# Optimization experiments

Measured on AMD Instinct MI355X. Metric: run time of the kernel, lower is better.

The kernel has to match this reference:

```python
import jax, jax.numpy as jnp
import numpy as np
import math

B, S, DIM = 1, 2048, 2048
H, KVH, HD = 32, 8, 64
REP = H // KVH


def _rope_cache(seqlen, head_dim, base=10000.0):
    # (seqlen, 2*head_dim): [cos | sin], each duplicated across both halves
    inv_freq = 1.0 / (base ** (np.arange(0, head_dim, 2, dtype=np.float32) / head_dim))
    t = np.arange(seqlen, dtype=np.float32)
    ang = np.outer(t, inv_freq)                    # (S, HD/2)
    ang = np.concatenate([ang, ang], axis=-1)      # (S, HD)
    return jnp.asarray(np.concatenate([np.cos(ang), np.sin(ang)], axis=-1))


def setup_inputs() -> dict:
    key = jax.random.key(0)
    ks = jax.random.split(key, 12)
    std = 0.02
    return {
        "x": jax.random.normal(ks[0], (B, S, DIM), jnp.float32),
        "rope_cache": _rope_cache(S, HD),
        "wq_w": jax.random.normal(ks[1], (H * HD, DIM), jnp.float32) * std,
        "wq_b": jax.random.normal(ks[2], (H * HD,), jnp.float32) * std,
        "wk_w": jax.random.normal(ks[3], (KVH * HD, DIM), jnp.float32) * std,
        "wk_b": jax.random.normal(ks[4], (KVH * HD,), jnp.float32) * std,
        "wv_w": jax.random.normal(ks[5], (KVH * HD, DIM), jnp.float32) * std,
        "wv_b": jax.random.normal(ks[6], (KVH * HD,), jnp.float32) * std,
        "wo_w": jax.random.normal(ks[7], (DIM, H * HD), jnp.float32) * std,
        "wo_b": jax.random.normal(ks[8], (DIM,), jnp.float32) * std,
        "sinks": jax.random.normal(ks[9], (H,), jnp.float32) * std,
    }


def _rotate_half(t):
    h = t.shape[-1] // 2
    return jnp.concatenate([-t[..., h:], t[..., :h]], axis=-1)


def reference(x, rope_cache, wq_w, wq_b, wk_w, wk_b, wv_w, wv_b, wo_w, wo_b, sinks):
    bsz, seqlen, _ = x.shape
    q = (jnp.einsum('bsd,od->bso', x, wq_w) + wq_b).reshape(bsz, seqlen, H, HD)
    k = (jnp.einsum('bsd,od->bso', x, wk_w) + wk_b).reshape(bsz, seqlen, KVH, HD)
    v = (jnp.einsum('bsd,od->bso', x, wv_w) + wv_b).reshape(bsz, seqlen, KVH, HD)

    cos = rope_cache[:seqlen, :HD][None, :, None, :]
    sin = rope_cache[:seqlen, HD:][None, :, None, :]
    q = q * cos + _rotate_half(q) * sin
    k = k * cos + _rotate_half(k) * sin

    # repeat_kv: repeat_interleave along head dim
    k = jnp.repeat(k, REP, axis=2)  # (B,S,H,HD)
    v = jnp.repeat(v, REP, axis=2)

    q = q.transpose(0, 2, 1, 3)  # (B,H,S,HD)
    k = k.transpose(0, 2, 1, 3)
    v = v.transpose(0, 2, 1, 3)

    scale = 1.0 / math.sqrt(HD)
    scores = jnp.einsum('bhqd,bhkd->bhqk', q, k) * scale
    causal = jnp.tril(jnp.ones((seqlen, seqlen), dtype=bool))
    scores = jnp.where(causal, scores, -jnp.inf)

    m = jnp.max(scores, axis=-1, keepdims=True)
    lse = m[..., 0] + jnp.log(jnp.sum(jnp.exp(scores - m), axis=-1))  # (B,H,S)
    attn = jnp.exp(scores - lse[..., None])
    out = jnp.einsum('bhqk,bhkd->bhqd', attn, v)

    # sink-token LSE renormalization
    combined_lse = jnp.logaddexp(lse, sinks[None, :, None])
    renorm = jnp.exp(jnp.clip(lse - combined_lse, -20.0, 0.0))
    out = out * renorm[..., None]

    out = out.transpose(0, 2, 1, 3).reshape(bsz, seqlen, H * HD)
    return jnp.einsum('bso,do->bsd', out, wo_w) + wo_b
```

## Files before the change

### kernel.cpp

```cpp
#include <hip/hip_runtime.h>


#define S_LEN 2048
#define DIM_  2048
#define QK_LD 2560

typedef __attribute__((ext_vector_type(8))) __bf16 bf16x8;
typedef __attribute__((ext_vector_type(4))) float f32x4;
typedef __attribute__((ext_vector_type(4))) unsigned short us4;

__device__ __forceinline__ unsigned short f2bf(float f) {
    union { float f; unsigned u; } v; v.f = f;
    unsigned r = v.u + 0x7FFFu + ((v.u >> 16) & 1u);
    return (unsigned short)(r >> 16);
}
__device__ __forceinline__ float bf2f(unsigned short u) {
    union { unsigned u; float f; } v; v.u = ((unsigned)u) << 16;
    return v.f;
}

__device__ __forceinline__ void gload_lds16(const void* g, void* l) {
    __builtin_amdgcn_global_load_lds(
        (const __attribute__((address_space(1))) void*)g,
        (__attribute__((address_space(3))) void*)l, 16, 0, 0);
}

__device__ __forceinline__ int swz32(int r, int ch) { return r*32 + ((ch ^ ((r >> 1) & 3)) << 3); }
__device__ __forceinline__ int swz64(int r, int ch) { return r*64 + ((ch ^ (r & 7)) << 3); }

__global__ void cvt_all(const float* __restrict__ x,  const float* __restrict__ wq,
                        const float* __restrict__ wk, const float* __restrict__ wv,
                        const float* __restrict__ wo,
                        unsigned short* __restrict__ xb,
                        unsigned short* __restrict__ wqkv,
                        unsigned short* __restrict__ wob) {
    const int i4 = blockIdx.x * 256 + threadIdx.x;
    const float* src; unsigned short* dst; int off;
    if (i4 < 1048576)      { src = x;  dst = xb;             off = i4; }
    else if (i4 < 2097152) { src = wq; dst = wqkv;           off = i4 - 1048576; }
    else if (i4 < 2359296) { src = wk; dst = wqkv + 4194304; off = i4 - 2097152; }
    else if (i4 < 2621440) { src = wv; dst = wqkv + 5242880; off = i4 - 2359296; }
    else                   { src = wo; dst = wob;            off = i4 - 2621440; }
    const float4 v = reinterpret_cast<const float4*>(src)[off];
    us4 o = { f2bf(v.x), f2bf(v.y), f2bf(v.z), f2bf(v.w) };
    reinterpret_cast<us4*>(dst)[off] = o;
}

__global__ void build_bias(const float* __restrict__ qb, const float* __restrict__ kb,
                           const float* __restrict__ vb, float* __restrict__ out) {
    const int i = blockIdx.x * 256 + threadIdx.x;
    if (i < 2048) out[i] = qb[i];
    else if (i < 2560) out[i] = kb[i - 2048];
    else if (i < 3072) out[i] = vb[i - 2560];
}

template<int MODE>
__global__ __launch_bounds__(256)
void gemm_bt(const unsigned short* __restrict__ A,
             const unsigned short* __restrict__ B,
             const float* __restrict__ bias,
             unsigned short* __restrict__ Cqk,
             unsigned short* __restrict__ Vt,
             float* __restrict__ Cf,
             int K)
{
    __shared__ unsigned short As[3][128 * 32];
    __shared__ unsigned short Bs[3][128 * 32];
    const int t = threadIdx.x;
    const int lane = t & 63;
    const int w = t >> 6;
    const int wr = w >> 1, wc = w & 1;
    const int lq = lane & 15;
    const int g = lane >> 4;
    const int m0 = blockIdx.y * 128;
    const int n0 = blockIdx.x * 128;

    const f32x4 z = {0.f, 0.f, 0.f, 0.f};
    f32x4 acc[4][4];
    #pragma unroll
    for (int i = 0; i < 4; i++)
        #pragma unroll
        for (int j = 0; j < 4; j++) acc[i][j] = z;

    auto stage = [&](int buf, int k0) {
        #pragma unroll
        for (int c = 0; c < 2; c++) {
            const int chunk = w * 128 + c * 64 + lane;
            const int r = chunk >> 2;
            const int chl = (chunk & 3) ^ ((r >> 1) & 3);
            gload_lds16(&A[(size_t)(m0 + r) * K + k0 + (chl << 3)],
                        &As[buf][(size_t)(w * 128 + c * 64) * 8]);
            gload_lds16(&B[(size_t)(n0 + r) * K + k0 + (chl << 3)],
                        &Bs[buf][(size_t)(w * 128 + c * 64) * 8]);
        }
    };

    const int NIT = K >> 5;
    stage(0, 0);
    stage(1, 32);
    for (int it = 0; it < NIT; ++it) {
        if (it + 1 < NIT) asm volatile("s_waitcnt vmcnt(4)" ::: "memory");
        else              asm volatile("s_waitcnt vmcnt(0)" ::: "memory");
        __builtin_amdgcn_s_barrier();
        if (it + 2 < NIT) stage((it + 2) % 3, (it + 2) << 5);
        const int cur = it % 3;
        bf16x8 a[4], b[4];
        #pragma unroll
        for (int mi = 0; mi < 4; mi++)
            a[mi] = *reinterpret_cast<const bf16x8*>(&As[cur][swz32(wr * 64 + mi * 16 + lq, g)]);
        #pragma unroll
        for (int ni = 0; ni < 4; ni++)
            b[ni] = *reinterpret_cast<const bf16x8*>(&Bs[cur][swz32(wc * 64 + ni * 16 + lq, g)]);
        #pragma unroll
        for (int mi = 0; mi < 4; mi++)
            #pragma unroll
            for (int ni = 0; ni < 4; ni++)
                acc[mi][ni] = __builtin_amdgcn_mfma_f32_16x16x32_bf16(a[mi], b[ni], acc[mi][ni], 0, 0, 0);
    }

    #pragma unroll
    for (int mi = 0; mi < 4; mi++) {
        const int row0 = m0 + wr * 64 + mi * 16 + g * 4;
        #pragma unroll
        for (int ni = 0; ni < 4; ni++) {
            const int col = n0 + wc * 64 + ni * 16 + lq;
            const float bv = bias[col];
            if (MODE == 1) {
                #pragma unroll
                for (int j = 0; j < 4; j++)
                    Cf[(size_t)(row0 + j) * 2048 + col] = acc[mi][ni][j] + bv;
            } else {
                if (col < 2560) {
                    const float qs = (col < 2048) ? 0.1803368801f : 1.0f;
                    #pragma unroll
                    for (int j = 0; j < 4; j++)
                        Cqk[(size_t)(row0 + j) * QK_LD + col] = f2bf((acc[mi][ni][j] + bv) * qs);
                } else {
                    us4 pk;
                    #pragma unroll
                    for (int j = 0; j < 4; j++) pk[j] = f2bf(acc[mi][ni][j] + bv);
                    *reinterpret_cast<us4*>(&Vt[(size_t)(col - 2560) * S_LEN + row0]) = pk;
                }
            }
        }
    }
}

__global__ void rope_kernel(unsigned short* __restrict__ qk, const float* __restrict__ rope) {
    const int idx = blockIdx.x * 256 + threadIdx.x;
    const int s = idx / 1280;
    const int rem = idx - s * 1280;
    const int head = rem >> 5;
    const int p = rem & 31;
    const size_t base = (size_t)s * QK_LD + head * 64 + p;
    const float c = rope[s * 128 + p];
    const float sn = rope[s * 128 + 64 + p];
    const float x0 = bf2f(qk[base]);
    const float x1 = bf2f(qk[base + 32]);
    qk[base]      = f2bf(x0 * c - x1 * sn);
    qk[base + 32] = f2bf(x1 * c + x0 * sn);
}

__global__ __launch_bounds__(256)
void attn_kernel(const unsigned short* __restrict__ qk,
                 const unsigned short* __restrict__ vt,
                 unsigned short* __restrict__ pacc,
                 float* __restrict__ pml)
{
    const int bx = blockIdx.x;
    const int c = bx & 1;
    const int qb = 31 - (bx >> 1);
    const int h = blockIdx.y;
    const int hkv = h >> 2;
    const int t = threadIdx.x;
    const int lane = t & 63;
    const int w = t >> 6;
    const int lq = lane & 15;
    const int g = lane >> 4;

    __shared__ unsigned short Ks[2][64 * 64];
    __shared__ unsigned short Vs[2][64 * 64];
    __shared__ unsigned short Ps[4][16 * 64];
    unsigned short* Pw = &Ps[w][0];

    const int qrow = qb * 64 + w * 16 + lq;

    bf16x8 aq[2];
    #pragma unroll
    for (int cc = 0; cc < 2; cc++)
        aq[cc] = *reinterpret_cast<const bf16x8*>(&qk[(size_t)qrow * QK_LD + h * 64 + cc * 32 + g * 8]);
    {
        const uint4 u0 = reinterpret_cast<const uint4&>(aq[0]);
        const uint4 u1 = reinterpret_cast<const uint4&>(aq[1]);
        asm volatile("" :: "v"(u0.x), "v"(u0.y), "v"(u0.z), "v"(u0.w),
                           "v"(u1.x), "v"(u1.y), "v"(u1.z), "v"(u1.w));
    }

    const f32x4 z = {0.f, 0.f, 0.f, 0.f};
    f32x4 acc[4];
    #pragma unroll
    for (int df = 0; df < 4; df++) acc[df] = z;
    float m = -1e30f, l = 0.f;

    auto stage = [&](int buf, int tv) {
        const int kv0 = tv * 64;
        #pragma unroll
        for (int i = 0; i < 2; i++) {
            const int chunk = i * 256 + w * 64 + lane;
            const int r = chunk >> 3;
            const int chl = (chunk & 7) ^ (r & 7);
            gload_lds16(&qk[(size_t)(kv0 + r) * QK_LD + 2048 + hkv * 64 + (chl << 3)],
                        &Ks[buf][(size_t)(i * 256 + w * 64) * 8]);
            gload_lds16(&vt[(size_t)(hkv * 64 + r) * S_LEN + kv0 + (chl << 3)],
                        &Vs[buf][(size_t)(i * 256 + w * 64) * 8]);
        }
    };

    const int ntile = (qb >= c) ? ((qb - c) >> 1) + 1 : 0;
    if (ntile > 0) stage(0, c);
    int cur = 0;
    for (int i = 0; i < ntile; ++i) {
        const int tv = c + 2 * i;
        asm volatile("s_waitcnt vmcnt(0)" ::: "memory");
        __builtin_amdgcn_s_barrier();
        if (i + 1 < ntile) stage(cur ^ 1, tv + 2);

        f32x4 sc[4];
        #pragma unroll
        for (int f = 0; f < 4; f++) {
            sc[f] = z;
            #pragma unroll
            for (int cc = 0; cc < 2; cc++) {
                const bf16x8 bk = *reinterpret_cast<const bf16x8*>(&Ks[cur][swz64(f * 16 + lq, cc * 4 + g)]);
                sc[f] = __builtin_amdgcn_mfma_f32_16x16x32_bf16(bk, aq[cc], sc[f], 0, 0, 0);
            }
        }

        if (tv == qb) {
            const int thr = w * 16 + lq - g * 4;
            #pragma unroll
            for (int f = 0; f < 4; f++)
                #pragma unroll
                for (int j = 0; j < 4; j++)
                    if (f * 16 + j > thr) sc[f][j] = -1e30f;
        }

        float mx = sc[0][0];
        #pragma unroll
        for (int f = 0; f < 4; f++)
            #pragma unroll
            for (int j = 0; j < 4; j++) mx = fmaxf(mx, sc[f][j]);
        mx = fmaxf(mx, __shfl_xor(mx, 16));
        mx = fmaxf(mx, __shfl_xor(mx, 32));
        const float mn = fmaxf(m, mx);
        const float rs = exp2f(m - mn);
        m = mn;
        float s = 0.f;
        #pragma unroll
        for (int f = 0; f < 4; f++)
            #pragma unroll
            for (int j = 0; j < 4; j++) {
                const float p = exp2f(sc[f][j] - mn);
                sc[f][j] = p;
                s += p;
            }
        s += __shfl_xor(s, 16);
        s += __shfl_xor(s, 32);
        l = l * rs + s;
        #pragma unroll
        for (int df = 0; df < 4; df++) acc[df] *= rs;

        #pragma unroll
        for (int f = 0; f < 4; f++) {
            us4 pk = { f2bf(sc[f][0]), f2bf(sc[f][1]), f2bf(sc[f][2]), f2bf(sc[f][3]) };
            *reinterpret_cast<us4*>(
                &Pw[lq * 64 + ((((f << 1) | (g >> 1)) ^ (lq & 7)) << 3) + ((g & 1) << 2)]) = pk;
        }
        #pragma unroll
        for (int cc = 0; cc < 2; cc++) {
            const bf16x8 pb = *reinterpret_cast<const bf16x8*>(
                &Pw[lq * 64 + (((cc * 4 + g) ^ (lq & 7)) << 3)]);
            #pragma unroll
            for (int df = 0; df < 4; df++) {
                const bf16x8 bv = *reinterpret_cast<const bf16x8*>(&Vs[cur][swz64(df * 16 + lq, cc * 4 + g)]);
                acc[df] = __builtin_amdgcn_mfma_f32_16x16x32_bf16(bv, pb, acc[df], 0, 0, 0);
            }
        }
        cur ^= 1;
    }

    const size_t rbase = ((size_t)(h * 2 + c) * 2048 + qrow);
    #pragma unroll
    for (int df = 0; df < 4; df++) {
        us4 pk = { f2bf(acc[df][0]), f2bf(acc[df][1]), f2bf(acc[df][2]), f2bf(acc[df][3]) };
        *reinterpret_cast<us4*>(&pacc[rbase * 64 + df * 16 + g * 4]) = pk;
    }
    if (g == 0) {
        pml[rbase * 2]     = m;
        pml[rbase * 2 + 1] = l;
    }
}

__global__ void attn_combine(const unsigned short* __restrict__ pacc,
                             const float* __restrict__ pml,
                             const float* __restrict__ sinks,
                             unsigned short* __restrict__ abuf) {
    const int idx = blockIdx.x * 256 + threadIdx.x;
    const int q4 = idx & 3;
    const int row = (idx >> 2) & 2047;
    const int h = idx >> 13;
    const size_t r0 = (size_t)(h * 2 + 0) * 2048 + row;
    const size_t r1 = (size_t)(h * 2 + 1) * 2048 + row;
    const float m0 = pml[r0 * 2], l0 = pml[r0 * 2 + 1];
    const float m1 = pml[r1 * 2], l1 = pml[r1 * 2 + 1];
    const float M = fmaxf(m0, m1);
    const float w0 = exp2f(m0 - M), w1 = exp2f(m1 - M);
    const float L = l0 * w0 + l1 * w1;
    const float lse = 0.6931471806f * (M + log2f(L));
    const float d = sinks[h] - lse;
    float f = (d > 20.f) ? d : log1pf(__expf(d));
    if (f > 20.f) f = 20.f;
    const float fac = __expf(-f) / L;
    const unsigned short* a0 = &pacc[r0 * 64 + q4 * 16];
    const unsigned short* a1 = &pacc[r1 * 64 + q4 * 16];
    unsigned short* dst = &abuf[(size_t)row * DIM_ + h * 64 + q4 * 16];
    #pragma unroll
    for (int k = 0; k < 4; k++) {
        const us4 x0 = *reinterpret_cast<const us4*>(&a0[k * 4]);
        const us4 x1 = *reinterpret_cast<const us4*>(&a1[k * 4]);
        us4 r;
        #pragma unroll
        for (int j = 0; j < 4; j++)
            r[j] = f2bf((bf2f(x0[j]) * w0 + bf2f(x1[j]) * w1) * fac);
        *reinterpret_cast<us4*>(&dst[k * 4]) = r;
    }
}

extern "C" void kernel_launch(void* const* d_in, const int* in_sizes, int n_in,
                              void* d_out, int out_size, void* d_ws, size_t ws_size,
                              hipStream_t stream) {
    const float* x     = (const float*)d_in[0];
    const float* rope  = (const float*)d_in[1];
    const float* wq_w  = (const float*)d_in[2];
    const float* wq_b  = (const float*)d_in[3];
    const float* wk_w  = (const float*)d_in[4];
    const float* wk_b  = (const float*)d_in[5];
    const float* wv_w  = (const float*)d_in[6];
    const float* wv_b  = (const float*)d_in[7];
    const float* wo_w  = (const float*)d_in[8];
    const float* wo_b  = (const float*)d_in[9];
    const float* sinks = (const float*)d_in[10];
    float* out = (float*)d_out;

    char* ws = (char*)d_ws;
    unsigned short* xb    = (unsigned short*)(ws);
    unsigned short* wqkv  = (unsigned short*)(ws + (8u  << 20));
    unsigned short* wob   = (unsigned short*)(ws + (20u << 20));
    unsigned short* qkbuf = (unsigned short*)(ws + (28u << 20));
    unsigned short* vtbuf = (unsigned short*)(ws + (38u << 20));
    unsigned short* abuf  = (unsigned short*)(ws + (40u << 20));
    float*          bcat  = (float*)(ws + (48u << 20));
    unsigned short* pacc  = (unsigned short*)(ws);
    float*          pml   = (float*)(ws + (16u << 20));

    cvt_all<<<14336, 256, 0, stream>>>(x, wq_w, wk_w, wv_w, wo_w, xb, wqkv, wob);
    build_bias<<<12, 256, 0, stream>>>(wq_b, wk_b, wv_b, bcat);

    gemm_bt<0><<<dim3(24, 16), 256, 0, stream>>>(xb, wqkv, bcat, qkbuf, vtbuf, nullptr, 2048);
    rope_kernel<<<10240, 256, 0, stream>>>(qkbuf, rope);
    attn_kernel<<<dim3(64, 32), 256, 0, stream>>>(qkbuf, vtbuf, pacc, pml);
    attn_combine<<<1024, 256, 0, stream>>>(pacc, pml, sinks, abuf);
    gemm_bt<1><<<dim3(16, 16), 256, 0, stream>>>(abuf, wob, wo_b, nullptr, nullptr, out, 2048);
}
```

Before: 288.0 us.

## Split-K GEMMs with bf16 partials and separate bias/rope/combine kernels

Both projection GEMMs are split along K into two halves (grid z=2). Each half writes bf16 partial products, and new combine kernels sum the partials, add bias, and apply RoPE and the Q scale, or transpose V. The aim is more blocks to fill the GPU, since 384 and 256 tiles underfill it. The cost is extra partial-buffer traffic, extra launches, and an extra bf16 rounding on the partials that may hurt accuracy. The change also drops the pipeline from three LDS buffers to two with a full vmcnt(0) wait, swaps the attention grid axes so heads vary fastest, and uses the native bf16 convert.

```diff
diff --git a/kernel.cpp b/kernel.cpp
--- a/kernel.cpp
+++ b/kernel.cpp
@@ -10,9 +10,8 @@
 typedef __attribute__((ext_vector_type(4))) unsigned short us4;
 
 __device__ __forceinline__ unsigned short f2bf(float f) {
-    union { float f; unsigned u; } v; v.f = f;
-    unsigned r = v.u + 0x7FFFu + ((v.u >> 16) & 1u);
-    return (unsigned short)(r >> 16);
+    const __bf16 h = (__bf16)f;
+    return __builtin_bit_cast(unsigned short, h);
 }
 __device__ __forceinline__ float bf2f(unsigned short u) {
     union { unsigned u; float f; } v; v.u = ((unsigned)u) << 16;
@@ -54,18 +53,14 @@
     else if (i < 3072) out[i] = vb[i - 2560];
 }
 
-template<int MODE>
 __global__ __launch_bounds__(256)
-void gemm_bt(const unsigned short* __restrict__ A,
-             const unsigned short* __restrict__ B,
-             const float* __restrict__ bias,
-             unsigned short* __restrict__ Cqk,
-             unsigned short* __restrict__ Vt,
-             float* __restrict__ Cf,
-             int K)
+void gemm_part(const unsigned short* __restrict__ A,
+               const unsigned short* __restrict__ B,
+               unsigned short* __restrict__ P,
+               int K, int ldc)
 {
-    __shared__ unsigned short As[3][128 * 32];
-    __shared__ unsigned short Bs[3][128 * 32];
+    __shared__ unsigned short As[2][128 * 32];
+    __shared__ unsigned short Bs[2][128 * 32];
     const int t = threadIdx.x;
     const int lane = t & 63;
     const int w = t >> 6;
@@ -74,6 +69,8 @@
     const int g = lane >> 4;
     const int m0 = blockIdx.y * 128;
     const int n0 = blockIdx.x * 128;
+    const int kbase = blockIdx.z * (K >> 1);
+    const size_t zoff = (size_t)blockIdx.z * 2048 * ldc;
 
     const f32x4 z = {0.f, 0.f, 0.f, 0.f};
     f32x4 acc[4][4];
@@ -88,22 +85,20 @@
             const int chunk = w * 128 + c * 64 + lane;
             const int r = chunk >> 2;
             const int chl = (chunk & 3) ^ ((r >> 1) & 3);
-            gload_lds16(&A[(size_t)(m0 + r) * K + k0 + (chl << 3)],
+            gload_lds16(&A[(size_t)(m0 + r) * K + kbase + k0 + (chl << 3)],
                         &As[buf][(size_t)(w * 128 + c * 64) * 8]);
-            gload_lds16(&B[(size_t)(n0 + r) * K + k0 + (chl << 3)],
+            gload_lds16(&B[(size_t)(n0 + r) * K + kbase + k0 + (chl << 3)],
                         &Bs[buf][(size_t)(w * 128 + c * 64) * 8]);
         }
     };
 
-    const int NIT = K >> 5;
+    const int NIT = K >> 6;
     stage(0, 0);
-    stage(1, 32);
     for (int it = 0; it < NIT; ++it) {
-        if (it + 1 < NIT) asm volatile("s_waitcnt vmcnt(4)" ::: "memory");
-        else              asm volatile("s_waitcnt vmcnt(0)" ::: "memory");
+        const int cur = it & 1;
+        asm volatile("s_waitcnt vmcnt(0)" ::: "memory");
         __builtin_amdgcn_s_barrier();
-        if (it + 2 < NIT) stage((it + 2) % 3, (it + 2) << 5);
-        const int cur = it % 3;
+        if (it + 1 < NIT) stage(cur ^ 1, (it + 1) << 5);
         bf16x8 a[4], b[4];
         #pragma unroll
         for (int mi = 0; mi < 4; mi++)
@@ -124,41 +119,48 @@
         #pragma unroll
         for (int ni = 0; ni < 4; ni++) {
             const int col = n0 + wc * 64 + ni * 16 + lq;
-            const float bv = bias[col];
-            if (MODE == 1) {
-                #pragma unroll
-                for (int j = 0; j < 4; j++)
-                    Cf[(size_t)(row0 + j) * 2048 + col] = acc[mi][ni][j] + bv;
-            } else {
-                if (col < 2560) {
-                    const float qs = (col < 2048) ? 0.1803368801f : 1.0f;
-                    #pragma unroll
-                    for (int j = 0; j < 4; j++)
-                        Cqk[(size_t)(row0 + j) * QK_LD + col] = f2bf((acc[mi][ni][j] + bv) * qs);
-                } else {
-                    us4 pk;
-                    #pragma unroll
-                    for (int j = 0; j < 4; j++) pk[j] = f2bf(acc[mi][ni][j] + bv);
-                    *reinterpret_cast<us4*>(&Vt[(size_t)(col - 2560) * S_LEN + row0]) = pk;
-                }
-            }
-        }
-    }
-}
-
-__global__ void rope_kernel(unsigned short* __restrict__ qk, const float* __restrict__ rope) {
+            #pragma unroll
+            for (int j = 0; j < 4; j++)
+                P[zoff + (size_t)(row0 + j) * ldc + col] = f2bf(acc[mi][ni][j]);
+        }
+    }
+}
+
+__global__ void rope_combine(const unsigned short* __restrict__ pq,
+                             const float* __restrict__ bias,
+                             const float* __restrict__ rope,
+                             unsigned short* __restrict__ qk,
+                             unsigned short* __restrict__ vt)
+{
     const int idx = blockIdx.x * 256 + threadIdx.x;
-    const int s = idx / 1280;
-    const int rem = idx - s * 1280;
-    const int head = rem >> 5;
-    const int p = rem & 31;
-    const size_t base = (size_t)s * QK_LD + head * 64 + p;
-    const float c = rope[s * 128 + p];
-    const float sn = rope[s * 128 + 64 + p];
-    const float x0 = bf2f(qk[base]);
-    const float x1 = bf2f(qk[base + 32]);
-    qk[base]      = f2bf(x0 * c - x1 * sn);
-    qk[base + 32] = f2bf(x1 * c + x0 * sn);
+    if (idx < 2621440) {
+        const int s = idx / 1280;
+        const int rem = idx - s * 1280;
+        const int head = rem >> 5;
+        const int p = rem & 31;
+        const int col0 = head * 64 + p;
+        const int col1 = col0 + 32;
+        const size_t r0 = (size_t)s * 3072;
+        const float v0 = bf2f(pq[r0 + col0]) + bf2f(pq[6291456 + r0 + col0]) + bias[col0];
+        const float v1 = bf2f(pq[r0 + col1]) + bf2f(pq[6291456 + r0 + col1]) + bias[col1];
+        const float c = rope[s * 128 + p];
+        const float sn = rope[s * 128 + 64 + p];
+        const float qs = (head < 32) ? 0.1803368801f : 1.0f;
+        qk[(size_t)s * QK_LD + col0] = f2bf((v0 * c - v1 * sn) * qs);
+        qk[(size_t)s * QK_LD + col1] = f2bf((v1 * c + v0 * sn) * qs);
+    } else {
+        const int i = idx - 2621440;
+        const int d = i >> 9;
+        const int s4 = (i & 511) << 2;
+        const float bv = bias[2560 + d];
+        us4 o;
+        #pragma unroll
+        for (int j = 0; j < 4; j++) {
+            const size_t r = (size_t)(s4 + j) * 3072 + 2560 + d;
+            o[j] = f2bf(bf2f(pq[r]) + bf2f(pq[6291456 + r]) + bv);
+        }
+        *reinterpret_cast<us4*>(&vt[(size_t)d * S_LEN + s4]) = o;
+    }
 }
 
 __global__ __launch_bounds__(256)
@@ -167,10 +169,10 @@
                  unsigned short* __restrict__ pacc,
                  float* __restrict__ pml)
 {
-    const int bx = blockIdx.x;
-    const int c = bx & 1;
-    const int qb = 31 - (bx >> 1);
-    const int h = blockIdx.y;
+    const int h = blockIdx.x;
+    const int by = blockIdx.y;
+    const int c = by & 1;
+    const int qb = 31 - (by >> 1);
     const int hkv = h >> 2;
     const int t = threadIdx.x;
     const int lane = t & 63;
@@ -336,6 +338,23 @@
     }
 }
 
+__global__ void o_combine(const unsigned short* __restrict__ po,
+                          const float* __restrict__ ob,
+                          float* __restrict__ out) {
+    const int idx = blockIdx.x * 256 + threadIdx.x;
+    const int row = idx >> 9;
+    const int c4 = (idx & 511) << 2;
+    float4 o;
+    const size_t r = (size_t)row * 2048 + c4;
+    const us4 x0 = *reinterpret_cast<const us4*>(&po[r]);
+    const us4 x1 = *reinterpret_cast<const us4*>(&po[4194304 + r]);
+    o.x = bf2f(x0[0]) + bf2f(x1[0]) + ob[c4];
+    o.y = bf2f(x0[1]) + bf2f(x1[1]) + ob[c4 + 1];
+    o.z = bf2f(x0[2]) + bf2f(x1[2]) + ob[c4 + 2];
+    o.w = bf2f(x0[3]) + bf2f(x1[3]) + ob[c4 + 3];
+    *reinterpret_cast<float4*>(&out[r]) = o;
+}
+
 extern "C" void kernel_launch(void* const* d_in, const int* in_sizes, int n_in,
                               void* d_out, int out_size, void* d_ws, size_t ws_size,
                               hipStream_t stream) {
@@ -356,19 +375,22 @@
     unsigned short* xb    = (unsigned short*)(ws);
     unsigned short* wqkv  = (unsigned short*)(ws + (8u  << 20));
     unsigned short* wob   = (unsigned short*)(ws + (20u << 20));
-    unsigned short* qkbuf = (unsigned short*)(ws + (28u << 20));
-    unsigned short* vtbuf = (unsigned short*)(ws + (38u << 20));
-    unsigned short* abuf  = (unsigned short*)(ws + (40u << 20));
-    float*          bcat  = (float*)(ws + (48u << 20));
-    unsigned short* pacc  = (unsigned short*)(ws);
-    float*          pml   = (float*)(ws + (16u << 20));
+    unsigned short* pq    = (unsigned short*)(ws + (28u << 20));
+    unsigned short* qkbuf = (unsigned short*)(ws);
+    unsigned short* vtbuf = (unsigned short*)(ws + (10u << 20));
+    unsigned short* pacc  = (unsigned short*)(ws + (28u << 20));
+    float*          pml   = (float*)(ws + (44u << 20));
+    unsigned short* abuf  = (unsigned short*)(ws + (46u << 20));
+    unsigned short* po    = (unsigned short*)(ws);
+    float*          bcat  = (float*)(ws + (54u << 20));
 
     cvt_all<<<14336, 256, 0, stream>>>(x, wq_w, wk_w, wv_w, wo_w, xb, wqkv, wob);
     build_bias<<<12, 256, 0, stream>>>(wq_b, wk_b, wv_b, bcat);
 
-    gemm_bt<0><<<dim3(24, 16), 256, 0, stream>>>(xb, wqkv, bcat, qkbuf, vtbuf, nullptr, 2048);
-    rope_kernel<<<10240, 256, 0, stream>>>(qkbuf, rope);
-    attn_kernel<<<dim3(64, 32), 256, 0, stream>>>(qkbuf, vtbuf, pacc, pml);
+    gemm_part<<<dim3(24, 16, 2), 256, 0, stream>>>(xb, wqkv, pq, 2048, 3072);
+    rope_combine<<<11264, 256, 0, stream>>>(pq, bcat, rope, qkbuf, vtbuf);
+    attn_kernel<<<dim3(32, 64), 256, 0, stream>>>(qkbuf, vtbuf, pacc, pml);
     attn_combine<<<1024, 256, 0, stream>>>(pacc, pml, sinks, abuf);
-    gemm_bt<1><<<dim3(16, 16), 256, 0, stream>>>(abuf, wob, wo_b, nullptr, nullptr, out, 2048);
-}
+    gemm_part<<<dim3(16, 16, 2), 256, 0, stream>>>(abuf, wob, po, 2048, 2048);
+    o_combine<<<4096, 256, 0, stream>>>(po, wo_b, out);
+}
```

Result: faster. 252.6 us (-12.3%).
